# Kernel optimization log

Measured on AMD Instinct MI355X. Metric: run time of the kernel, lower is better.

The kernel has to match this reference:

```python
import jax, jax.numpy as jnp
import numpy as np
from functools import partial

N_ITER = 200  # LML(n_iter=200)


def sq_dists(Xi, x):
    # Xi: [N, n], x: [B, n] -> squared euclidean dists [B, N] (torch.cdist ** 2)
    x2 = jnp.sum(x * x, axis=1, keepdims=True)          # [B, 1]
    m2 = jnp.sum(Xi * Xi, axis=1)                        # [N]
    d = x2 + m2[None, :] - 2.0 * (x @ Xi.T)
    return jnp.maximum(d, 0.0)


def _lml_solve(x, k):
    # LML projection: y = sigmoid(x + nu), nu s.t. sum(y) = k; bisection on nu.
    x_sorted = -jnp.sort(-x, axis=1)                     # descending
    lo = -x_sorted[:, k - 1] - 7.0
    hi = -x_sorted[:, k] + 7.0

    def body(i, bounds):
        lo, hi = bounds
        mid = 0.5 * (lo + hi)
        f = jnp.sum(jax.nn.sigmoid(x + mid[:, None]), axis=1) - k
        lo = jnp.where(f < 0, mid, lo)
        hi = jnp.where(f < 0, hi, mid)
        return lo, hi

    lo, hi = jax.lax.fori_loop(0, N_ITER, body, (lo, hi))
    nu = 0.5 * (lo + hi)
    return jax.nn.sigmoid(x + nu[:, None])


@partial(jax.custom_vjp, nondiff_argnums=(1,))
def lml(x, k):
    return _lml_solve(x, k)


def _lml_fwd(x, k):
    y = _lml_solve(x, k)
    return y, y


def _lml_bwd(k, y, g):
    # implicit grad: dy = s*(dx - dnu), dnu = sum(s*dx)/sum(s), s = y(1-y)
    s = y * (1.0 - y)
    dnu = jnp.sum(s * g, axis=1, keepdims=True) / jnp.sum(s, axis=1, keepdims=True)
    return (s * (g - dnu),)


lml.defvjp(_lml_fwd, _lml_bwd)


def k_softmax(beta, x, k):
    # x: [B, N] (= -dists) -> [B, N, k]
    cols = [jax.nn.softmax(beta * x, axis=1)]
    last = cols[0]
    for i in range(1, k):
        new = lml(beta * x, i + 1)
        cols.append(new - last)
        last = new
    return jnp.stack(cols, axis=2)


def hopfield(Xi, x, beta):
    return jax.nn.softmax(-beta * sq_dists(Xi, x), axis=1) @ Xi


def k_hopfield_batch(Xi, x, k, beta, hopfield_steps):
    dists = sq_dists(Xi, x)                              # [B, N]
    ksm = k_softmax(beta, -dists, k)                     # [B, N, k]
    result = jnp.einsum('nd,bnk->bdk', Xi, ksm)          # Xi.T @ ksm -> [B, n, k]
    for _ in range(hopfield_steps):
        result = jnp.stack(
            [hopfield(Xi, result[:, :, j], beta) for j in range(k)], axis=2)
    return result


def setup_inputs() -> dict:
    key = jax.random.key(0)
    kx, km = jax.random.split(key)
    return {
        'x': jax.random.normal(kx, (2048, 512), dtype=jnp.float32),
        'memories': jax.random.normal(km, (8192, 512), dtype=jnp.float32),
        'k': 5,
        'beta': 1,
        'hopfield_steps': 2,
    }


def reference(x, memories, k, beta, hopfield_steps):
    return k_hopfield_batch(memories, x, k, beta, hopfield_steps)
```

## Files before the change

kernel.cpp:

```cpp
#include <hip/hip_runtime.h>
#include <hip/hip_bf16.h>


constexpr int   Bq    = 2048;
constexpr int   Nm    = 8192;
constexpr int   Dd    = 512;
constexpr int   KK    = 5;
constexpr float BETA  = 1.0f;
constexpr int   STEPS = 2;
constexpr int   KS    = 8;
constexpr size_t PL   = (size_t)Bq * Dd;

#define DEV static __device__ __forceinline__

typedef __attribute__((ext_vector_type(8))) short           short8v;
typedef __attribute__((ext_vector_type(8))) unsigned short  u16x8;
typedef __attribute__((ext_vector_type(4))) float           f32x4;

DEV float b2f(ushort u) { unsigned v = ((unsigned)u) << 16; float f; __builtin_memcpy(&f, &v, 4); return f; }
DEV ushort f2b(float f) { __hip_bfloat16 h = __float2bfloat16(f); ushort u; __builtin_memcpy(&u, &h, 2); return u; }
DEV float ldin(const void* p, int isf, size_t idx) {
    return isf ? ((const float*)p)[idx] : b2f(((const ushort*)p)[idx]);
}

__global__ __launch_bounds__(256) void detect_k(const ushort* __restrict__ xin,
                                                int* __restrict__ flag) {
    __shared__ int sb;
    if (threadIdx.x == 0) sb = 0;
    __syncthreads();
    int bad = 0;
    for (int i = threadIdx.x; i < 1024; i += 256) {
        float v = b2f(xin[i]);
        if (!(fabsf(v) < 64.0f)) bad = 1;
    }
    if (bad) atomicOr(&sb, 1);
    __syncthreads();
    if (threadIdx.x == 0) flag[0] = sb;
}

__global__ __launch_bounds__(256) void norms_k(const void* __restrict__ xin,
                                               const void* __restrict__ memin,
                                               const int* __restrict__ flag,
                                               float* __restrict__ x2,
                                               float* __restrict__ m2) {
    int row = blockIdx.x;
    int isf = flag[0];
    const void* src; size_t base; float* dst;
    if (row < Nm) { src = memin; base = (size_t)row * Dd; dst = m2 + row; }
    else          { src = xin; base = (size_t)(row - Nm) * Dd; dst = x2 + (row - Nm); }
    int tid = threadIdx.x, lane = tid & 63, wave = tid >> 6;
    float s = 0.f;
    for (int i = tid; i < Dd; i += 256) { float v = ldin(src, isf, base + i); s += v * v; }
    for (int off = 32; off; off >>= 1) s += __shfl_down(s, off, 64);
    __shared__ float ws[4];
    if (lane == 0) ws[wave] = s;
    __syncthreads();
    if (tid == 0) dst[0] = ws[0] + ws[1] + ws[2] + ws[3];
}


__global__ __launch_bounds__(256) void convHL_k(const void* __restrict__ src,
                                                const int* __restrict__ flag,
                                                ushort* __restrict__ H,
                                                ushort* __restrict__ L,
                                                int nQuads, int qoff) {
    int isf = flag[0];
    for (int i = blockIdx.x * 256 + threadIdx.x; i < nQuads; i += gridDim.x * 256) {
        float v[4];
        if (isf) {
            float4 t = ((const float4*)src)[qoff + i];
            v[0] = t.x; v[1] = t.y; v[2] = t.z; v[3] = t.w;
        } else {
            ushort4 t = ((const ushort4*)src)[qoff + i];
            v[0] = b2f(t.x); v[1] = b2f(t.y); v[2] = b2f(t.z); v[3] = b2f(t.w);
        }
        ushort4 h, l;
        ushort* hp = (ushort*)&h; ushort* lp = (ushort*)&l;
#pragma unroll
        for (int j = 0; j < 4; ++j) {
            ushort hu = f2b(v[j]);
            hp[j] = hu;
            lp[j] = f2b(v[j] - b2f(hu));
        }
        ((ushort4*)H)[i] = h;
        ((ushort4*)L)[i] = l;
    }
}

__global__ __launch_bounds__(256) void convT_k(const void* __restrict__ memin,
                                               const int* __restrict__ flag,
                                               ushort* __restrict__ TH,
                                               ushort* __restrict__ TL) {
    __shared__ float tile[64][65];
    const int isf = flag[0];
    const int n0 = blockIdx.x * 64, d0 = blockIdx.y * 64;
    const int tid = threadIdx.x;
    {
        const int r = tid >> 2, cseg = tid & 3;
#pragma unroll
        for (int j = 0; j < 16; ++j)
            tile[r][cseg * 16 + j] = ldin(memin, isf, (size_t)(n0 + r) * Dd + d0 + cseg * 16 + j);
    }
    __syncthreads();
    {
        const int drow = tid >> 2, nseg = tid & 3;
        u16x8 h[2], l[2];
#pragma unroll
        for (int c = 0; c < 2; ++c)
#pragma unroll
            for (int j = 0; j < 8; ++j) {
                float v = tile[nseg * 16 + c * 8 + j][drow];
                ushort hu = f2b(v);
                h[c][j] = hu;
                l[c][j] = f2b(v - b2f(hu));
            }
        size_t base = (size_t)(d0 + drow) * Nm + n0 + nseg * 16;
#pragma unroll
        for (int c = 0; c < 2; ++c) {
            *(u16x8*)&TH[base + c * 8] = h[c];
            *(u16x8*)&TL[base + c * 8] = l[c];
        }
    }
}

__global__ __launch_bounds__(256) void distMF2_k(const ushort* __restrict__ Ah,
                                                 const ushort* __restrict__ Al,
                                                 const ushort* __restrict__ Mh,
                                                 const ushort* __restrict__ Ml,
                                                 float* __restrict__ S,
                                                 const float* __restrict__ a2,
                                                 const float* __restrict__ m2,
                                                 int ab0, float negBeta) {
    __shared__ ushort TA[2][4][128][8];
    __shared__ ushort TB[2][4][128][8];
    const int tid = threadIdx.x, lane = tid & 63, wid = tid >> 6;
    const int wm = wid >> 1, wn = wid & 1;
    const int m0 = blockIdx.y * 128, n0 = blockIdx.x * 128;
    const int srow = tid & 127, kb = tid >> 7;
    const size_t baseA = (size_t)(ab0 + m0 + srow) * Dd;
    const size_t baseB = (size_t)(n0 + srow) * Dd;

    f32x4 acc[4][4];
    const f32x4 z = {0.f, 0.f, 0.f, 0.f};
#pragma unroll
    for (int i = 0; i < 4; ++i)
#pragma unroll
        for (int j = 0; j < 4; ++j) acc[i][j] = z;

    for (int k0 = 0; k0 < Dd; k0 += 32) {
        u16x8 rah0 = *(const u16x8*)&Ah[baseA + k0 + kb * 8];
        u16x8 rah1 = *(const u16x8*)&Ah[baseA + k0 + (kb + 2) * 8];
        u16x8 ral0 = *(const u16x8*)&Al[baseA + k0 + kb * 8];
        u16x8 ral1 = *(const u16x8*)&Al[baseA + k0 + (kb + 2) * 8];
        u16x8 rbh0 = *(const u16x8*)&Mh[baseB + k0 + kb * 8];
        u16x8 rbh1 = *(const u16x8*)&Mh[baseB + k0 + (kb + 2) * 8];
        u16x8 rbl0 = *(const u16x8*)&Ml[baseB + k0 + kb * 8];
        u16x8 rbl1 = *(const u16x8*)&Ml[baseB + k0 + (kb + 2) * 8];
        __syncthreads();
        *(u16x8*)&TA[0][kb][srow][0]     = rah0;
        *(u16x8*)&TA[0][kb + 2][srow][0] = rah1;
        *(u16x8*)&TA[1][kb][srow][0]     = ral0;
        *(u16x8*)&TA[1][kb + 2][srow][0] = ral1;
        *(u16x8*)&TB[0][kb][srow][0]     = rbh0;
        *(u16x8*)&TB[0][kb + 2][srow][0] = rbh1;
        *(u16x8*)&TB[1][kb][srow][0]     = rbl0;
        *(u16x8*)&TB[1][kb + 2][srow][0] = rbl1;
        __syncthreads();

        const int rl = lane & 15, kc = lane >> 4;
        short8v ah[4], al[4];
#pragma unroll
        for (int fm = 0; fm < 4; ++fm) {
            const int ra_ = wm * 64 + fm * 16 + rl;
            ah[fm] = *(const short8v*)&TA[0][kc][ra_][0];
            al[fm] = *(const short8v*)&TA[1][kc][ra_][0];
        }
#pragma unroll
        for (int fn = 0; fn < 4; ++fn) {
            const int rb_ = wn * 64 + fn * 16 + rl;
            short8v bh = *(const short8v*)&TB[0][kc][rb_][0];
            short8v bl = *(const short8v*)&TB[1][kc][rb_][0];
#pragma unroll
            for (int fm = 0; fm < 4; ++fm) {
                acc[fm][fn] = __builtin_amdgcn_mfma_f32_16x16x32_bf16(ah[fm], bh, acc[fm][fn], 0, 0, 0);
                acc[fm][fn] = __builtin_amdgcn_mfma_f32_16x16x32_bf16(al[fm], bh, acc[fm][fn], 0, 0, 0);
                acc[fm][fn] = __builtin_amdgcn_mfma_f32_16x16x32_bf16(ah[fm], bl, acc[fm][fn], 0, 0, 0);
            }
        }
    }

    const int col = lane & 15, r0 = (lane >> 4) * 4;
#pragma unroll
    for (int fm = 0; fm < 4; ++fm)
#pragma unroll
        for (int fn = 0; fn < 4; ++fn) {
            const int n = n0 + wn * 64 + fn * 16 + col;
            const float mm2 = m2[n];
#pragma unroll
            for (int q = 0; q < 4; ++q) {
                const int m = m0 + wm * 64 + fm * 16 + r0 + q;
                const float d = a2[m] + mm2 - 2.0f * acc[fm][fn][q];
                S[(size_t)m * Nm + n] = negBeta * fmaxf(d, 0.0f);
            }
        }
}

__global__ __launch_bounds__(256) void wconv_k(const float* __restrict__ S,
                                               const float* __restrict__ par6,
                                               const float* __restrict__ par2,
                                               ushort* __restrict__ Wh,
                                               ushort* __restrict__ Wl,
                                               int mode, int jj) {
    const int b = blockIdx.x, tid = threadIdx.x;
    float p0 = 0.f, p1 = 0.f;
    if (mode == 0)      { p0 = par6[b * 6 + 0]; p1 = 1.0f / par6[b * 6 + 1]; }
    else if (mode == 1) { p0 = par6[b * 6 + 1 + jj]; }
    else                { p0 = par2[b * 2 + 0]; p1 = par2[b * 2 + 1]; }
    const float4* sp = (const float4*)(S + (size_t)b * Nm);
    ushort* whp = Wh + (size_t)b * Nm;
    ushort* wlp = Wl + (size_t)b * Nm;
#pragma unroll
    for (int r = 0; r < 8; ++r) {
        const int qi = r * 256 + tid;
        float4 t = sp[qi];
        float s4[4] = {t.x, t.y, t.z, t.w};
        ushort4 oh, ol;
        ushort* ohp = (ushort*)&oh;
        ushort* olp = (ushort*)&ol;
#pragma unroll
        for (int j = 0; j < 4; ++j) {
            float w;
            if (mode == 1) w = 1.0f / (1.0f + expf(-(s4[j] + p0)));
            else           w = expf(s4[j] - p0) * p1;
            ushort hu = f2b(w);
            ohp[j] = hu;
            olp[j] = f2b(w - b2f(hu));
        }
        ((ushort4*)whp)[qi] = oh;
        ((ushort4*)wlp)[qi] = ol;
    }
}

__global__ __launch_bounds__(256) void wgemm3_k(const ushort* __restrict__ Wh,
                                                const ushort* __restrict__ Wl,
                                                const ushort* __restrict__ MTh,
                                                const ushort* __restrict__ MTl,
                                                float* __restrict__ part,
                                                int planeSz, int nzLen) {
    __shared__ ushort TW[2][4][128][8];
    __shared__ ushort TB[2][4][64][8];
    const int tid = threadIdx.x, lane = tid & 63, wid = tid >> 6;
    const int wm = wid >> 1, wn = wid & 1;
    const int d0 = blockIdx.x * 64, b0 = blockIdx.y * 128;
    const int nz0 = blockIdx.z * nzLen;

    const int wrow = tid & 127, wkb = tid >> 7;
    const int brow = tid & 63,  bkc = tid >> 6;
    const size_t baseW = (size_t)(b0 + wrow) * Nm;
    const size_t baseB = (size_t)(d0 + brow) * Nm;

    f32x4 acc[4][2];
    const f32x4 z = {0.f, 0.f, 0.f, 0.f};
#pragma unroll
    for (int i = 0; i < 4; ++i)
#pragma unroll
        for (int j = 0; j < 2; ++j) acc[i][j] = z;

    for (int nc = nz0; nc < nz0 + nzLen; nc += 32) {
        u16x8 rwh0 = *(const u16x8*)&Wh[baseW + nc + wkb * 8];
        u16x8 rwh1 = *(const u16x8*)&Wh[baseW + nc + (wkb + 2) * 8];
        u16x8 rwl0 = *(const u16x8*)&Wl[baseW + nc + wkb * 8];
        u16x8 rwl1 = *(const u16x8*)&Wl[baseW + nc + (wkb + 2) * 8];
        u16x8 rbh  = *(const u16x8*)&MTh[baseB + nc + bkc * 8];
        u16x8 rbl  = *(const u16x8*)&MTl[baseB + nc + bkc * 8];
        __syncthreads();
        *(u16x8*)&TW[0][wkb][wrow][0]     = rwh0;
        *(u16x8*)&TW[0][wkb + 2][wrow][0] = rwh1;
        *(u16x8*)&TW[1][wkb][wrow][0]     = rwl0;
        *(u16x8*)&TW[1][wkb + 2][wrow][0] = rwl1;
        *(u16x8*)&TB[0][bkc][brow][0]     = rbh;
        *(u16x8*)&TB[1][bkc][brow][0]     = rbl;
        __syncthreads();

        const int rl = lane & 15, kc = lane >> 4;
        short8v wfh[4], wfl[4];
#pragma unroll
        for (int fm = 0; fm < 4; ++fm) {
            const int rw_ = wm * 64 + fm * 16 + rl;
            wfh[fm] = *(const short8v*)&TW[0][kc][rw_][0];
            wfl[fm] = *(const short8v*)&TW[1][kc][rw_][0];
        }
#pragma unroll
        for (int fn = 0; fn < 2; ++fn) {
            const int rd_ = wn * 32 + fn * 16 + rl;
            short8v bh = *(const short8v*)&TB[0][kc][rd_][0];
            short8v bl = *(const short8v*)&TB[1][kc][rd_][0];
#pragma unroll
            for (int fm = 0; fm < 4; ++fm) {
                acc[fm][fn] = __builtin_amdgcn_mfma_f32_16x16x32_bf16(wfh[fm], bh, acc[fm][fn], 0, 0, 0);
                acc[fm][fn] = __builtin_amdgcn_mfma_f32_16x16x32_bf16(wfl[fm], bh, acc[fm][fn], 0, 0, 0);
                acc[fm][fn] = __builtin_amdgcn_mfma_f32_16x16x32_bf16(wfh[fm], bl, acc[fm][fn], 0, 0, 0);
            }
        }
    }

    float* pz = part + (size_t)blockIdx.z * planeSz;
    const int col = lane & 15, r0 = (lane >> 4) * 4;
#pragma unroll
    for (int fm = 0; fm < 4; ++fm)
#pragma unroll
        for (int fn = 0; fn < 2; ++fn) {
            const int dc = d0 + wn * 32 + fn * 16 + col;
#pragma unroll
            for (int q = 0; q < 4; ++q) {
                const int br = b0 + wm * 64 + fm * 16 + r0 + q;
                pz[(size_t)br * Dd + dc] = acc[fm][fn][q];
            }
        }
}

__global__ __launch_bounds__(256) void reduceHL_k(const float* __restrict__ part,
                                                  ushort* __restrict__ Rh,
                                                  ushort* __restrict__ Rl,
                                                  float* __restrict__ r2w, int doNorm,
                                                  int planeSz, int ks) {
    int row = blockIdx.x, tid = threadIdx.x, lane = tid & 63, wave = tid >> 6;
    float sq = 0.f;
    for (int e = tid; e < Dd; e += 256) {
        float s = 0.f;
        for (int z = 0; z < ks; ++z) s += part[(size_t)z * planeSz + (size_t)row * Dd + e];
        ushort h = f2b(s);
        Rh[(size_t)row * Dd + e] = h;
        Rl[(size_t)row * Dd + e] = f2b(s - b2f(h));
        sq += s * s;
    }
    if (doNorm) {
        for (int off = 32; off; off >>= 1) sq += __shfl_down(sq, off, 64);
        __shared__ float ws[4];
        if (lane == 0) ws[wave] = sq;
        __syncthreads();
        if (tid == 0) r2w[row] = ws[0] + ws[1] + ws[2] + ws[3];
    }
}

__global__ __launch_bounds__(256) void combineHL_k(ushort* __restrict__ rhl,
                                                   float* __restrict__ r2all) {
    int row = blockIdx.x, tid = threadIdx.x, lane = tid & 63, wave = tid >> 6;
    float sq[5] = {0.f, 0.f, 0.f, 0.f, 0.f};
    for (int e = tid; e < Dd; e += 256) {
        size_t idx = (size_t)row * Dd + e;
        float v[5];
#pragma unroll
        for (int j = 0; j < 5; ++j)
            v[j] = b2f(rhl[(size_t)j * 2 * PL + idx]) + b2f(rhl[(size_t)j * 2 * PL + PL + idx]);
        float o[5];
        o[0] = v[0];
        o[1] = v[1] - v[0]; o[2] = v[2] - v[1]; o[3] = v[3] - v[2]; o[4] = v[4] - v[3];
#pragma unroll
        for (int j = 1; j < 5; ++j) {
            ushort h = f2b(o[j]);
            rhl[(size_t)j * 2 * PL + idx] = h;
            rhl[(size_t)j * 2 * PL + PL + idx] = f2b(o[j] - b2f(h));
        }
#pragma unroll
        for (int j = 0; j < 5; ++j) sq[j] += o[j] * o[j];
    }
    __shared__ float ws[5][4];
#pragma unroll
    for (int j = 0; j < 5; ++j) {
        float s = sq[j];
        for (int off = 32; off; off >>= 1) s += __shfl_down(s, off, 64);
        if (lane == 0) ws[j][wave] = s;
    }
    __syncthreads();
    if (tid < 5) r2all[tid * Bq + row] = ws[tid][0] + ws[tid][1] + ws[tid][2] + ws[tid][3];
}

__global__ __launch_bounds__(256) void finalHL_k(const ushort* __restrict__ rhl,
                                                 void* __restrict__ out,
                                                 const int* __restrict__ flag) {
    size_t idx = (size_t)blockIdx.x * 256 + threadIdx.x;
    bool isf = flag[0] != 0;
#pragma unroll
    for (int j = 0; j < KK; ++j) {
        float v = b2f(rhl[(size_t)j * 2 * PL + idx]) + b2f(rhl[(size_t)j * 2 * PL + PL + idx]);
        if (isf) ((float*)out)[idx * KK + j] = v;
        else     ((ushort*)out)[idx * KK + j] = f2b(v);
    }
}


__global__ __launch_bounds__(256) void rowstats_k(const float* __restrict__ S,
                                                  float* __restrict__ stats) {
    int b = blockIdx.x, tid = threadIdx.x, lane = tid & 63, wave = tid >> 6;
    __shared__ float cbuf[1024];
    __shared__ int   ccnt;
    __shared__ float tops[256 * 6];
    __shared__ float stop[6];
    __shared__ float wred[16];
    __shared__ float bcast[5];
    const float* srow = S + (size_t)b * Nm;

    float tt[6];
#pragma unroll
    for (int q = 0; q < 6; ++q) tt[q] = -3.4e38f;
    for (int i = tid; i < Nm; i += 256) {
        float v = srow[i];
        if (v > tt[5]) {
            tt[5] = v;
#pragma unroll
            for (int q = 5; q > 0; --q)
                if (tt[q] > tt[q - 1]) { float tm = tt[q]; tt[q] = tt[q - 1]; tt[q - 1] = tm; }
        }
    }
#pragma unroll
    for (int q = 0; q < 6; ++q) tops[tid * 6 + q] = tt[q];
    if (tid == 0) ccnt = 0;
    __syncthreads();
    if (tid == 0) {
        float mt[6];
#pragma unroll
        for (int q = 0; q < 6; ++q) mt[q] = -3.4e38f;
        for (int i = 0; i < 256 * 6; ++i) {
            float v = tops[i];
            if (v > mt[5]) {
                mt[5] = v;
#pragma unroll
                for (int q = 5; q > 0; --q)
                    if (mt[q] > mt[q - 1]) { float tm = mt[q]; mt[q] = mt[q - 1]; mt[q - 1] = tm; }
            }
        }
#pragma unroll
        for (int q = 0; q < 6; ++q) stop[q] = mt[q];
    }
    __syncthreads();

    float smax = stop[0];
    float cutoff = stop[5] - 40.0f;
    float p = 0.f;
    for (int i = tid; i < Nm; i += 256) {
        float v = srow[i];
        p += expf(v - smax);
        if (v >= cutoff) {
            int idx = atomicAdd(&ccnt, 1);
            if (idx < 1024) cbuf[idx] = v;
        }
    }
    for (int off = 32; off; off >>= 1) p += __shfl_down(p, off, 64);
    if (lane == 0) wred[wave] = p;
    __syncthreads();
    if (tid == 0) bcast[4] = wred[0] + wred[1] + wred[2] + wred[3];
    __syncthreads();
    float denom = bcast[4];
    int cnt = min(ccnt, 1024);

    float lo[4], hi[4];
#pragma unroll
// ... 99 lines not shown
            int r = c >> 4, k = c & 15;
            As[k][r] = ldin(A, isfA, (size_t)(ab0 + m0 + r) * Dd + d0 + k);
            Bs[k][r] = ldin(memin, isfB, (size_t)(n0 + r) * Dd + d0 + k);
        }
        __syncthreads();
#pragma unroll
        for (int k = 0; k < 16; ++k) {
            float4 av = *(const float4*)&As[k][ty * 4];
            float4 bv = *(const float4*)&Bs[k][tx * 4];
            float a[4] = {av.x, av.y, av.z, av.w};
            float b[4] = {bv.x, bv.y, bv.z, bv.w};
#pragma unroll
            for (int i = 0; i < 4; ++i)
#pragma unroll
                for (int j = 0; j < 4; ++j) acc[i][j] = fmaf(a[i], b[j], acc[i][j]);
        }
        __syncthreads();
    }
#pragma unroll
    for (int i = 0; i < 4; ++i) {
        int m = m0 + ty * 4 + i;
        float4 o;
        float* po = (float*)&o;
#pragma unroll
        for (int j = 0; j < 4; ++j) {
            float d = a2[m] + m2[n0 + tx * 4 + j] - 2.0f * acc[i][j];
            po[j] = negBeta * fmaxf(d, 0.0f);
        }
        *(float4*)&S[(size_t)m * Nm + n0 + tx * 4] = o;
    }
}

template <int TRF>
__global__ __launch_bounds__(256) void wgemmG_k(const float* __restrict__ Sx,
                                                const void* __restrict__ memin,
                                                const int* __restrict__ flag,
                                                const float* __restrict__ rowpar,
                                                float* __restrict__ part, int planeSz) {
    __shared__ float Ws[16][68];
    __shared__ float Bs[16][68];
    const int tid = threadIdx.x, tx = tid & 15, ty = tid >> 4;
    const int d0 = blockIdx.x * 64, b0 = blockIdx.y * 64;
    const int kz = blockIdx.z * (Nm / KS);
    const int isf = flag[0];

    float acc[4][4];
#pragma unroll
    for (int i = 0; i < 4; ++i)
#pragma unroll
        for (int j = 0; j < 4; ++j) acc[i][j] = 0.f;

    for (int nc = kz; nc < kz + Nm / KS; nc += 16) {
#pragma unroll
        for (int c = tid; c < 1024; c += 256) {
            int r = c >> 4, k = c & 15;
            float s = Sx[(size_t)(b0 + r) * Nm + nc + k];
            float p0 = rowpar[(b0 + r) * 2 + 0];
            float w;
            if constexpr (TRF == 1) w = expf(s - p0) * rowpar[(b0 + r) * 2 + 1];
            else                    w = 1.0f / (1.0f + expf(-(s + p0)));
            Ws[k][r] = w;
            int kk = c >> 6, dd = c & 63;
            Bs[kk][dd] = ldin(memin, isf, (size_t)(nc + kk) * Dd + d0 + dd);
        }
        __syncthreads();
#pragma unroll
        for (int k = 0; k < 16; ++k) {
            float4 av = *(const float4*)&Ws[k][ty * 4];
            float4 bv = *(const float4*)&Bs[k][tx * 4];
            float a[4] = {av.x, av.y, av.z, av.w};
            float b[4] = {bv.x, bv.y, bv.z, bv.w};
#pragma unroll
            for (int i = 0; i < 4; ++i)
#pragma unroll
                for (int j = 0; j < 4; ++j) acc[i][j] = fmaf(a[i], b[j], acc[i][j]);
        }
        __syncthreads();
    }
    float* pz = part + (size_t)blockIdx.z * planeSz;
#pragma unroll
    for (int i = 0; i < 4; ++i) {
        float4 o = {acc[i][0], acc[i][1], acc[i][2], acc[i][3]};
        *(float4*)&pz[(size_t)(b0 + ty * 4 + i) * Dd + d0 + tx * 4] = o;
    }
}

__global__ __launch_bounds__(256) void reduceN_k(const float* __restrict__ part,
                                                 float* __restrict__ Rj,
                                                 float* __restrict__ r2w, int doNorm,
                                                 int planeSz) {
    int row = blockIdx.x, tid = threadIdx.x, lane = tid & 63, wave = tid >> 6;
    float sq = 0.f;
    for (int e = tid; e < Dd; e += 256) {
        float s = 0.f;
#pragma unroll
        for (int z = 0; z < KS; ++z) s += part[(size_t)z * planeSz + (size_t)row * Dd + e];
        Rj[(size_t)row * Dd + e] = s;
        sq += s * s;
    }
    if (doNorm) {
        for (int off = 32; off; off >>= 1) sq += __shfl_down(sq, off, 64);
        __shared__ float ws[4];
        if (lane == 0) ws[wave] = sq;
        __syncthreads();
        if (tid == 0) r2w[row] = ws[0] + ws[1] + ws[2] + ws[3];
    }
}

__global__ __launch_bounds__(256) void combine_k(float* __restrict__ R,
                                                 float* __restrict__ r2all) {
    int row = blockIdx.x, tid = threadIdx.x, lane = tid & 63, wave = tid >> 6;
    float sq[5] = {0.f, 0.f, 0.f, 0.f, 0.f};
    for (int e = tid; e < Dd; e += 256) {
        size_t idx = (size_t)row * Dd + e;
        float r0 = R[idx], r1 = R[PL + idx], r2v = R[2 * PL + idx],
              r3 = R[3 * PL + idx], r4 = R[4 * PL + idx];
        float o1 = r1 - r0, o2 = r2v - r1, o3 = r3 - r2v, o4 = r4 - r3;
        R[PL + idx] = o1; R[2 * PL + idx] = o2; R[3 * PL + idx] = o3; R[4 * PL + idx] = o4;
        sq[0] += r0 * r0; sq[1] += o1 * o1; sq[2] += o2 * o2; sq[3] += o3 * o3; sq[4] += o4 * o4;
    }
    __shared__ float ws[5][4];
#pragma unroll
    for (int j = 0; j < 5; ++j) {
        float s = sq[j];
        for (int off = 32; off; off >>= 1) s += __shfl_down(s, off, 64);
        if (lane == 0) ws[j][wave] = s;
    }
    __syncthreads();
    if (tid < 5) r2all[tid * Bq + row] = ws[tid][0] + ws[tid][1] + ws[tid][2] + ws[tid][3];
}

__global__ __launch_bounds__(256) void final_k(const float* __restrict__ R,
                                               void* __restrict__ out,
                                               const int* __restrict__ flag) {
    size_t idx = (size_t)blockIdx.x * 256 + threadIdx.x;
    bool isf = flag[0] != 0;
#pragma unroll
    for (int j = 0; j < KK; ++j) {
        float v = R[(size_t)j * PL + idx];
        if (isf) ((float*)out)[idx * KK + j] = v;
        else     ((ushort*)out)[idx * KK + j] = f2b(v);
    }
}


extern "C" void kernel_launch(void* const* d_in, const int* in_sizes, int n_in,
                              void* d_out, int out_size, void* d_ws, size_t ws_size,
                              hipStream_t stream) {
    const void* xin   = d_in[0];
    const void* memin = d_in[1];

    const size_t MiB = 1048576ull, KiB = 1024ull;
    char* ws = (char*)d_ws;
    float* part = (float*)d_out;

    int BcF = 0, ksF = 0;
    {
        const int cb[10] = {1024, 512, 512, 256, 256, 256, 128, 128, 128, 128};
        const int ck[10] = {   8,  16,   8,  32,  16,   8,  64,  32,  16,   8};
        for (int i = 0; i < 10; ++i) {
            size_t need = 52 * MiB + 160 * KiB + (size_t)cb[i] * 64 * KiB;
            size_t needOut = (size_t)ck[i] * cb[i] * Dd * 4;
            if (need <= ws_size && needOut <= (size_t)out_size) { BcF = cb[i]; ksF = ck[i]; break; }
        }
    }

    if (BcF) {
        const int Bc = BcF, ks = ksF;
        ushort* rhl  = (ushort*)(ws + 0);
        ushort* mh   = (ushort*)(ws + 20 * MiB);
        ushort* ml   = (ushort*)(ws + 28 * MiB);
        ushort* mth  = (ushort*)(ws + 36 * MiB);
        ushort* mtl  = (ushort*)(ws + 44 * MiB);
        char*  misc  = ws + 52 * MiB;
        float* m2    = (float*)(misc + 0);
        float* x2    = (float*)(misc + 32 * KiB);
        float* stats = (float*)(misc + 40 * KiB);
        float* rpar  = (float*)(misc + 88 * KiB);
        int*   flag  = (int*)  (misc + 104 * KiB);
        float* r2all = (float*)(misc + 112 * KiB);
        ushort* Wh   = (ushort*)(ws + 52 * MiB + 160 * KiB);
        ushort* Wl   = Wh + (size_t)Bc * Nm;
        float* S     = (float*)(ws + 52 * MiB + 160 * KiB + (size_t)Bc * 32 * KiB);
        ushort* xsH  = Wh;
        ushort* xsL  = Wh + (size_t)Bc * Dd;

        const int nChunk = Bq / Bc;
        const int planeSz = Bc * Dd;
        const int nzLen = Nm / ks;

        detect_k<<<1, 256, 0, stream>>>((const ushort*)xin, flag);
        norms_k<<<Nm + Bq, 256, 0, stream>>>(xin, memin, flag, x2, m2);
        convHL_k<<<2048, 256, 0, stream>>>(memin, flag, mh, ml, Nm * Dd / 4, 0);
        convT_k<<<dim3(Nm / 64, Dd / 64), 256, 0, stream>>>(memin, flag, mth, mtl);

        for (int c = 0; c < nChunk; ++c) {
            int b0 = c * Bc;
            convHL_k<<<Bc / 2, 256, 0, stream>>>(xin, flag, xsH, xsL,
                                                 Bc * Dd / 4, b0 * Dd / 4);
            distMF2_k<<<dim3(Nm / 128, Bc / 128), 256, 0, stream>>>(
                xsH, xsL, mh, ml, S, x2 + b0, m2, 0, -BETA);
            rowstats_k<<<Bc, 256, 0, stream>>>(S, stats + (size_t)b0 * 6);
            for (int jj = 0; jj < KK; ++jj) {
                wconv_k<<<Bc, 256, 0, stream>>>(S, stats + (size_t)b0 * 6, nullptr,
                                                Wh, Wl, jj == 0 ? 0 : 1, jj);
                wgemm3_k<<<dim3(Dd / 64, Bc / 128, ks), 256, 0, stream>>>(
                    Wh, Wl, mth, mtl, part, planeSz, nzLen);
                ushort* Rh = rhl + (size_t)jj * 2 * PL + (size_t)b0 * Dd;
                ushort* Rl = rhl + (size_t)jj * 2 * PL + PL + (size_t)b0 * Dd;
                reduceHL_k<<<Bc, 256, 0, stream>>>(part, Rh, Rl, nullptr, 0, planeSz, ks);
            }
        }
        combineHL_k<<<Bq, 256, 0, stream>>>(rhl, r2all);

        for (int st = 0; st < STEPS; ++st) {
            for (int jj = 0; jj < KK; ++jj) {
                ushort* Rhj = rhl + (size_t)jj * 2 * PL;
                ushort* Rlj = rhl + (size_t)jj * 2 * PL + PL;
                float* r2j = r2all + (size_t)jj * Bq;
                for (int c = 0; c < nChunk; ++c) {
                    int b0 = c * Bc;
                    distMF2_k<<<dim3(Nm / 128, Bc / 128), 256, 0, stream>>>(
                        Rhj, Rlj, mh, ml, S, r2j + b0, m2, b0, -BETA);
                    rowmax_denom_k<<<Bc, 256, 0, stream>>>(S, rpar + (size_t)b0 * 2);
                    wconv_k<<<Bc, 256, 0, stream>>>(S, nullptr, rpar + (size_t)b0 * 2,
                                                    Wh, Wl, 2, 0);
                    wgemm3_k<<<dim3(Dd / 64, Bc / 128, ks), 256, 0, stream>>>(
                        Wh, Wl, mth, mtl, part, planeSz, nzLen);
                    reduceHL_k<<<Bc, 256, 0, stream>>>(
                        part, Rhj + (size_t)b0 * Dd, Rlj + (size_t)b0 * Dd,
                        r2j + b0, 1, planeSz, ks);
                }
            }
        }
        finalHL_k<<<(int)(PL / 256), 256, 0, stream>>>(rhl, d_out, flag);
        return;
    }

    float* R     = (float*)(ws + 0);
    float* m2    = (float*)(ws + 20 * MiB);
    float* x2    = (float*)(ws + 20 * MiB + 32 * KiB);
    float* stats = (float*)(ws + 20 * MiB + 48 * KiB);
    float* rpar  = (float*)(ws + 20 * MiB + 96 * KiB);
    int*   flag  = (int*)  (ws + 20 * MiB + 112 * KiB);
    float* r2all = (float*)(ws + 20 * MiB + 128 * KiB);
    float* S     = (float*)(ws + 20 * MiB + 256 * KiB);

    int Bc = 128;
    const int cand[4] = {1024, 512, 256, 128};
    for (int i = 0; i < 4; ++i) {
        size_t needWS  = 20 * MiB + 256 * KiB + (size_t)cand[i] * Nm * 4;
        size_t needOut = (size_t)KS * cand[i] * Dd * 4;
        if (needWS <= ws_size && needOut <= (size_t)out_size) { Bc = cand[i]; break; }
    }
    const int nChunk = Bq / Bc;
    const int planeSz = Bc * Dd;

    detect_k<<<1, 256, 0, stream>>>((const ushort*)xin, flag);
    norms_k<<<Nm + Bq, 256, 0, stream>>>(xin, memin, flag, x2, m2);

    for (int c = 0; c < nChunk; ++c) {
        int b0 = c * Bc;
        distF2_k<<<dim3(Nm / 64, Bc / 64), 256, 0, stream>>>(
            xin, flag, 0, memin, S, x2 + b0, m2, b0, -BETA);
        rowstats_k<<<Bc, 256, 0, stream>>>(S, stats + (size_t)b0 * 6);
        for (int jj = 0; jj < KK; ++jj) {
            float* Rj = R + (size_t)jj * PL + (size_t)b0 * Dd;
            rowpar_stage1_k<<<Bq / 256, 256, 0, stream>>>(stats, rpar, jj);
            if (jj == 0)
                wgemmG_k<1><<<dim3(Dd / 64, Bc / 64, KS), 256, 0, stream>>>(
                    S, memin, flag, rpar + (size_t)b0 * 2, part, planeSz);
            else
                wgemmG_k<2><<<dim3(Dd / 64, Bc / 64, KS), 256, 0, stream>>>(
                    S, memin, flag, rpar + (size_t)b0 * 2, part, planeSz);
            reduceN_k<<<Bc, 256, 0, stream>>>(part, Rj, nullptr, 0, planeSz);
        }
    }
    combine_k<<<Bq, 256, 0, stream>>>(R, r2all);

    for (int st = 0; st < STEPS; ++st) {
        for (int jj = 0; jj < KK; ++jj) {
            float* Rj = R + (size_t)jj * PL;
            float* r2j = r2all + (size_t)jj * Bq;
            for (int c = 0; c < nChunk; ++c) {
                int b0 = c * Bc;
                distF2_k<<<dim3(Nm / 64, Bc / 64), 256, 0, stream>>>(
                    Rj, flag, 1, memin, S, r2j + b0, m2, b0, -BETA);
                rowmax_denom_k<<<Bc, 256, 0, stream>>>(S, rpar + (size_t)b0 * 2);
                wgemmG_k<1><<<dim3(Dd / 64, Bc / 64, KS), 256, 0, stream>>>(
                    S, memin, flag, rpar + (size_t)b0 * 2, part, planeSz);
                reduceN_k<<<Bc, 256, 0, stream>>>(
                    part, Rj + (size_t)b0 * Dd, r2j + b0, 1, planeSz);
            }
        }
    }
    final_k<<<(int)(PL / 256), 256, 0, stream>>>(R, d_out, flag);
}
```

Baseline: 11.67 ms.

## Convert memories to hi/lo bf16 inside dist GEMM and prefetch next tiles

The distance GEMM now reads the raw memory matrix (fp32 or bf16) and splits it into bf16 hi/lo parts in registers, so the precomputed mh/ml buffers and their conversion pass are gone. Both the distance GEMM and the weighted GEMM now issue global loads for the next k-tile right after the barrier, giving a register-level software prefetch. The workspace layout changes: the transposed memory planes move into the output buffer and the partial sums move into the workspace, with a new table of chunk and split sizes. The in-kernel conversion costs extra ALU work on every tile, and fp32 input doubles the bytes read for B.

```diff
diff --git a/kernel.cpp b/kernel.cpp
--- a/kernel.cpp
+++ b/kernel.cpp
@@ -123,10 +123,10 @@
     }
 }
 
-__global__ __launch_bounds__(256) void distMF2_k(const ushort* __restrict__ Ah,
+__global__ __launch_bounds__(256) void distMF3_k(const ushort* __restrict__ Ah,
                                                  const ushort* __restrict__ Al,
-                                                 const ushort* __restrict__ Mh,
-                                                 const ushort* __restrict__ Ml,
+                                                 const void* __restrict__ memin,
+                                                 const int* __restrict__ flag,
                                                  float* __restrict__ S,
                                                  const float* __restrict__ a2,
                                                  const float* __restrict__ m2,
@@ -136,6 +136,7 @@
     const int tid = threadIdx.x, lane = tid & 63, wid = tid >> 6;
     const int wm = wid >> 1, wn = wid & 1;
     const int m0 = blockIdx.y * 128, n0 = blockIdx.x * 128;
+    const int isf = flag[0];
     const int srow = tid & 127, kb = tid >> 7;
     const size_t baseA = (size_t)(ab0 + m0 + srow) * Dd;
     const size_t baseB = (size_t)(n0 + srow) * Dd;
@@ -147,25 +148,54 @@
 #pragma unroll
         for (int j = 0; j < 4; ++j) acc[i][j] = z;
 
+    u16x8 rah0, rah1, ral0, ral1;
+    float vb[16];
+
+    auto loadT = [&](int k0) {
+        rah0 = *(const u16x8*)&Ah[baseA + k0 + kb * 8];
+        rah1 = *(const u16x8*)&Ah[baseA + k0 + (kb + 2) * 8];
+        ral0 = *(const u16x8*)&Al[baseA + k0 + kb * 8];
+        ral1 = *(const u16x8*)&Al[baseA + k0 + (kb + 2) * 8];
+        if (isf) {
+            const float* mp = (const float*)memin + baseB + k0;
+            float4 t0 = *(const float4*)(mp + kb * 8);
+            float4 t1 = *(const float4*)(mp + kb * 8 + 4);
+            float4 t2 = *(const float4*)(mp + (kb + 2) * 8);
+            float4 t3 = *(const float4*)(mp + (kb + 2) * 8 + 4);
+            vb[0] = t0.x; vb[1] = t0.y; vb[2]  = t0.z; vb[3]  = t0.w;
+            vb[4] = t1.x; vb[5] = t1.y; vb[6]  = t1.z; vb[7]  = t1.w;
+            vb[8] = t2.x; vb[9] = t2.y; vb[10] = t2.z; vb[11] = t2.w;
+            vb[12] = t3.x; vb[13] = t3.y; vb[14] = t3.z; vb[15] = t3.w;
+        } else {
+            const ushort* mp = (const ushort*)memin + baseB + k0;
+            u16x8 t0 = *(const u16x8*)(mp + kb * 8);
+            u16x8 t1 = *(const u16x8*)(mp + (kb + 2) * 8);
+#pragma unroll
+            for (int j = 0; j < 8; ++j) { vb[j] = b2f(t0[j]); vb[8 + j] = b2f(t1[j]); }
+        }
+    };
+
+    loadT(0);
     for (int k0 = 0; k0 < Dd; k0 += 32) {
-        u16x8 rah0 = *(const u16x8*)&Ah[baseA + k0 + kb * 8];
-        u16x8 rah1 = *(const u16x8*)&Ah[baseA + k0 + (kb + 2) * 8];
-        u16x8 ral0 = *(const u16x8*)&Al[baseA + k0 + kb * 8];
-        u16x8 ral1 = *(const u16x8*)&Al[baseA + k0 + (kb + 2) * 8];
-        u16x8 rbh0 = *(const u16x8*)&Mh[baseB + k0 + kb * 8];
-        u16x8 rbh1 = *(const u16x8*)&Mh[baseB + k0 + (kb + 2) * 8];
-        u16x8 rbl0 = *(const u16x8*)&Ml[baseB + k0 + kb * 8];
-        u16x8 rbl1 = *(const u16x8*)&Ml[baseB + k0 + (kb + 2) * 8];
+        u16x8 h0, l0, h1, l1;
+#pragma unroll
+        for (int j = 0; j < 8; ++j) {
+            ushort hu = f2b(vb[j]);
+            h0[j] = hu; l0[j] = f2b(vb[j] - b2f(hu));
+            ushort hv = f2b(vb[8 + j]);
+            h1[j] = hv; l1[j] = f2b(vb[8 + j] - b2f(hv));
+        }
         __syncthreads();
         *(u16x8*)&TA[0][kb][srow][0]     = rah0;
         *(u16x8*)&TA[0][kb + 2][srow][0] = rah1;
         *(u16x8*)&TA[1][kb][srow][0]     = ral0;
         *(u16x8*)&TA[1][kb + 2][srow][0] = ral1;
-        *(u16x8*)&TB[0][kb][srow][0]     = rbh0;
-        *(u16x8*)&TB[0][kb + 2][srow][0] = rbh1;
-        *(u16x8*)&TB[1][kb][srow][0]     = rbl0;
-        *(u16x8*)&TB[1][kb + 2][srow][0] = rbl1;
-        __syncthreads();
+        *(u16x8*)&TB[0][kb][srow][0]     = h0;
+        *(u16x8*)&TB[0][kb + 2][srow][0] = h1;
+        *(u16x8*)&TB[1][kb][srow][0]     = l0;
+        *(u16x8*)&TB[1][kb + 2][srow][0] = l1;
+        __syncthreads();
+        if (k0 + 32 < Dd) loadT(k0 + 32);
 
         const int rl = lane & 15, kc = lane >> 4;
         short8v ah[4], al[4];
@@ -266,13 +296,18 @@
 #pragma unroll
         for (int j = 0; j < 2; ++j) acc[i][j] = z;
 
+    u16x8 rwh0, rwh1, rwl0, rwl1, rbh, rbl;
+    auto loadT = [&](int nc) {
+        rwh0 = *(const u16x8*)&Wh[baseW + nc + wkb * 8];
+        rwh1 = *(const u16x8*)&Wh[baseW + nc + (wkb + 2) * 8];
+        rwl0 = *(const u16x8*)&Wl[baseW + nc + wkb * 8];
+        rwl1 = *(const u16x8*)&Wl[baseW + nc + (wkb + 2) * 8];
+        rbh  = *(const u16x8*)&MTh[baseB + nc + bkc * 8];
+        rbl  = *(const u16x8*)&MTl[baseB + nc + bkc * 8];
+    };
+
+    loadT(nz0);
     for (int nc = nz0; nc < nz0 + nzLen; nc += 32) {
-        u16x8 rwh0 = *(const u16x8*)&Wh[baseW + nc + wkb * 8];
-        u16x8 rwh1 = *(const u16x8*)&Wh[baseW + nc + (wkb + 2) * 8];
-        u16x8 rwl0 = *(const u16x8*)&Wl[baseW + nc + wkb * 8];
-        u16x8 rwl1 = *(const u16x8*)&Wl[baseW + nc + (wkb + 2) * 8];
-        u16x8 rbh  = *(const u16x8*)&MTh[baseB + nc + bkc * 8];
-        u16x8 rbl  = *(const u16x8*)&MTl[baseB + nc + bkc * 8];
         __syncthreads();
         *(u16x8*)&TW[0][wkb][wrow][0]     = rwh0;
         *(u16x8*)&TW[0][wkb + 2][wrow][0] = rwh1;
@@ -281,6 +316,7 @@
         *(u16x8*)&TB[0][bkc][brow][0]     = rbh;
         *(u16x8*)&TB[1][bkc][brow][0]     = rbl;
         __syncthreads();
+        if (nc + 32 < nz0 + nzLen) loadT(nc + 32);
 
         const int rl = lane & 15, kc = lane >> 4;
         short8v wfh[4], wfl[4];
@@ -708,36 +744,36 @@
 
     const size_t MiB = 1048576ull, KiB = 1024ull;
     char* ws = (char*)d_ws;
-    float* part = (float*)d_out;
-
+
+    const size_t memTbytes = 2ull * Dd * Nm * 2;
     int BcF = 0, ksF = 0;
-    {
-        const int cb[10] = {1024, 512, 512, 256, 256, 256, 128, 128, 128, 128};
-        const int ck[10] = {   8,  16,   8,  32,  16,   8,  64,  32,  16,   8};
-        for (int i = 0; i < 10; ++i) {
-            size_t need = 52 * MiB + 160 * KiB + (size_t)cb[i] * 64 * KiB;
-            size_t needOut = (size_t)ck[i] * cb[i] * Dd * 4;
-            if (need <= ws_size && needOut <= (size_t)out_size) { BcF = cb[i]; ksF = ck[i]; break; }
+    if ((size_t)out_size >= memTbytes) {
+        const int cb[6] = {512, 512, 256, 256, 128, 128};
+        const int ck[6] = {  8,   4,  16,   8,  32,   8};
+        for (int i = 0; i < 6; ++i) {
+            size_t need = 20 * MiB + 160 * KiB
+                        + (size_t)cb[i] * 64 * KiB
+                        + (size_t)ck[i] * cb[i] * 2 * KiB;
+            if (need <= ws_size) { BcF = cb[i]; ksF = ck[i]; break; }
         }
     }
 
     if (BcF) {
         const int Bc = BcF, ks = ksF;
         ushort* rhl  = (ushort*)(ws + 0);
-        ushort* mh   = (ushort*)(ws + 20 * MiB);
-        ushort* ml   = (ushort*)(ws + 28 * MiB);
-        ushort* mth  = (ushort*)(ws + 36 * MiB);
-        ushort* mtl  = (ushort*)(ws + 44 * MiB);
-        char*  misc  = ws + 52 * MiB;
+        char*  misc  = ws + 20 * MiB;
         float* m2    = (float*)(misc + 0);
         float* x2    = (float*)(misc + 32 * KiB);
         float* stats = (float*)(misc + 40 * KiB);
         float* rpar  = (float*)(misc + 88 * KiB);
         int*   flag  = (int*)  (misc + 104 * KiB);
         float* r2all = (float*)(misc + 112 * KiB);
-        ushort* Wh   = (ushort*)(ws + 52 * MiB + 160 * KiB);
+        ushort* Wh   = (ushort*)(ws + 20 * MiB + 160 * KiB);
         ushort* Wl   = Wh + (size_t)Bc * Nm;
-        float* S     = (float*)(ws + 52 * MiB + 160 * KiB + (size_t)Bc * 32 * KiB);
+        float* S     = (float*)(ws + 20 * MiB + 160 * KiB + (size_t)Bc * 32 * KiB);
+        float* part  = (float*)(ws + 20 * MiB + 160 * KiB + (size_t)Bc * 64 * KiB);
+        ushort* mth  = (ushort*)d_out;
+        ushort* mtl  = mth + (size_t)Dd * Nm;
         ushort* xsH  = Wh;
         ushort* xsL  = Wh + (size_t)Bc * Dd;
 
@@ -747,15 +783,14 @@
 
         detect_k<<<1, 256, 0, stream>>>((const ushort*)xin, flag);
         norms_k<<<Nm + Bq, 256, 0, stream>>>(xin, memin, flag, x2, m2);
-        convHL_k<<<2048, 256, 0, stream>>>(memin, flag, mh, ml, Nm * Dd / 4, 0);
         convT_k<<<dim3(Nm / 64, Dd / 64), 256, 0, stream>>>(memin, flag, mth, mtl);
 
         for (int c = 0; c < nChunk; ++c) {
             int b0 = c * Bc;
             convHL_k<<<Bc / 2, 256, 0, stream>>>(xin, flag, xsH, xsL,
                                                  Bc * Dd / 4, b0 * Dd / 4);
-            distMF2_k<<<dim3(Nm / 128, Bc / 128), 256, 0, stream>>>(
-                xsH, xsL, mh, ml, S, x2 + b0, m2, 0, -BETA);
+            distMF3_k<<<dim3(Nm / 128, Bc / 128), 256, 0, stream>>>(
+                xsH, xsL, memin, flag, S, x2 + b0, m2, 0, -BETA);
             rowstats_k<<<Bc, 256, 0, stream>>>(S, stats + (size_t)b0 * 6);
             for (int jj = 0; jj < KK; ++jj) {
                 wconv_k<<<Bc, 256, 0, stream>>>(S, stats + (size_t)b0 * 6, nullptr,
@@ -776,8 +811,8 @@
                 float* r2j = r2all + (size_t)jj * Bq;
                 for (int c = 0; c < nChunk; ++c) {
                     int b0 = c * Bc;
-                    distMF2_k<<<dim3(Nm / 128, Bc / 128), 256, 0, stream>>>(
-                        Rhj, Rlj, mh, ml, S, r2j + b0, m2, b0, -BETA);
+                    distMF3_k<<<dim3(Nm / 128, Bc / 128), 256, 0, stream>>>(
+                        Rhj, Rlj, memin, flag, S, r2j + b0, m2, b0, -BETA);
                     rowmax_denom_k<<<Bc, 256, 0, stream>>>(S, rpar + (size_t)b0 * 2);
                     wconv_k<<<Bc, 256, 0, stream>>>(S, nullptr, rpar + (size_t)b0 * 2,
                                                     Wh, Wl, 2, 0);
@@ -793,6 +828,7 @@
         return;
     }
 
+    float* part = (float*)d_out;
     float* R     = (float*)(ws + 0);
     float* m2    = (float*)(ws + 20 * MiB);
     float* x2    = (float*)(ws + 20 * MiB + 32 * KiB);
```

Result: slower. 26.16 ms (+124.2%).

## Fuse weight transform and hi/lo split into GEMM operand load

Applied to the files above, without the earlier changes.

Removes the separate wconv pass that turned score rows into bf16 hi/lo weight planes. The GEMM kernel now reads the fp32 scores directly and applies exp or sigmoid with per-row parameters before packing into shared memory. Workspace layout is also reorganized: the transposed memory planes move into the output buffer, and the batch chunk and split-K values are fixed at 512/8. The cost is more exp work inside the GEMM, repeated across the Dd/64 column blocks, and wider fp32 reads per tile.

```diff
diff --git a/kernel.cpp b/kernel.cpp
--- a/kernel.cpp
+++ b/kernel.cpp
@@ -66,22 +66,19 @@
                                                 int nQuads, int qoff) {
     int isf = flag[0];
     for (int i = blockIdx.x * 256 + threadIdx.x; i < nQuads; i += gridDim.x * 256) {
-        float v[4];
+        float v0, v1, v2, v3;
         if (isf) {
             float4 t = ((const float4*)src)[qoff + i];
-            v[0] = t.x; v[1] = t.y; v[2] = t.z; v[3] = t.w;
+            v0 = t.x; v1 = t.y; v2 = t.z; v3 = t.w;
         } else {
             ushort4 t = ((const ushort4*)src)[qoff + i];
-            v[0] = b2f(t.x); v[1] = b2f(t.y); v[2] = b2f(t.z); v[3] = b2f(t.w);
+            v0 = b2f(t.x); v1 = b2f(t.y); v2 = b2f(t.z); v3 = b2f(t.w);
         }
         ushort4 h, l;
-        ushort* hp = (ushort*)&h; ushort* lp = (ushort*)&l;
-#pragma unroll
-        for (int j = 0; j < 4; ++j) {
-            ushort hu = f2b(v[j]);
-            hp[j] = hu;
-            lp[j] = f2b(v[j] - b2f(hu));
-        }
+        h.x = f2b(v0); l.x = f2b(v0 - b2f(h.x));
+        h.y = f2b(v1); l.y = f2b(v1 - b2f(h.y));
+        h.z = f2b(v2); l.z = f2b(v2 - b2f(h.z));
+        h.w = f2b(v3); l.w = f2b(v3 - b2f(h.w));
         ((ushort4*)H)[i] = h;
         ((ushort4*)L)[i] = l;
     }
@@ -104,21 +101,19 @@
     __syncthreads();
     {
         const int drow = tid >> 2, nseg = tid & 3;
-        u16x8 h[2], l[2];
-#pragma unroll
-        for (int c = 0; c < 2; ++c)
+        size_t base = (size_t)(d0 + drow) * Nm + n0 + nseg * 16;
+#pragma unroll
+        for (int c = 0; c < 2; ++c) {
+            u16x8 h, l;
 #pragma unroll
             for (int j = 0; j < 8; ++j) {
                 float v = tile[nseg * 16 + c * 8 + j][drow];
                 ushort hu = f2b(v);
-                h[c][j] = hu;
-                l[c][j] = f2b(v - b2f(hu));
+                h[j] = hu;
+                l[j] = f2b(v - b2f(hu));
             }
-        size_t base = (size_t)(d0 + drow) * Nm + n0 + nseg * 16;
-#pragma unroll
-        for (int c = 0; c < 2; ++c) {
-            *(u16x8*)&TH[base + c * 8] = h[c];
-            *(u16x8*)&TL[base + c * 8] = l[c];
+            *(u16x8*)&TH[base + c * 8] = h;
+            *(u16x8*)&TL[base + c * 8] = l;
         }
     }
 }
@@ -205,44 +200,15 @@
         }
 }
 
-__global__ __launch_bounds__(256) void wconv_k(const float* __restrict__ S,
-                                               const float* __restrict__ par6,
-                                               const float* __restrict__ par2,
-                                               ushort* __restrict__ Wh,
-                                               ushort* __restrict__ Wl,
-                                               int mode, int jj) {
-    const int b = blockIdx.x, tid = threadIdx.x;
-    float p0 = 0.f, p1 = 0.f;
-    if (mode == 0)      { p0 = par6[b * 6 + 0]; p1 = 1.0f / par6[b * 6 + 1]; }
-    else if (mode == 1) { p0 = par6[b * 6 + 1 + jj]; }
-    else                { p0 = par2[b * 2 + 0]; p1 = par2[b * 2 + 1]; }
-    const float4* sp = (const float4*)(S + (size_t)b * Nm);
-    ushort* whp = Wh + (size_t)b * Nm;
-    ushort* wlp = Wl + (size_t)b * Nm;
-#pragma unroll
-    for (int r = 0; r < 8; ++r) {
-        const int qi = r * 256 + tid;
-        float4 t = sp[qi];
-        float s4[4] = {t.x, t.y, t.z, t.w};
-        ushort4 oh, ol;
-        ushort* ohp = (ushort*)&oh;
-        ushort* olp = (ushort*)&ol;
-#pragma unroll
-        for (int j = 0; j < 4; ++j) {
-            float w;
-            if (mode == 1) w = 1.0f / (1.0f + expf(-(s4[j] + p0)));
-            else           w = expf(s4[j] - p0) * p1;
-            ushort hu = f2b(w);
-            ohp[j] = hu;
-            olp[j] = f2b(w - b2f(hu));
-        }
-        ((ushort4*)whp)[qi] = oh;
-        ((ushort4*)wlp)[qi] = ol;
-    }
-}
-
-__global__ __launch_bounds__(256) void wgemm3_k(const ushort* __restrict__ Wh,
-                                                const ushort* __restrict__ Wl,
+template <int TRF>
+DEV float wtr(float s, float p0, float p1) {
+    if (TRF == 1) return expf(s - p0) * p1;
+    else          return 1.0f / (1.0f + expf(-(s + p0)));
+}
+
+template <int TRF>
+__global__ __launch_bounds__(256) void wgemmF_k(const float* __restrict__ Sx,
+                                                const float* __restrict__ rowpar,
                                                 const ushort* __restrict__ MTh,
                                                 const ushort* __restrict__ MTl,
                                                 float* __restrict__ part,
@@ -256,8 +222,10 @@
 
     const int wrow = tid & 127, wkb = tid >> 7;
     const int brow = tid & 63,  bkc = tid >> 6;
-    const size_t baseW = (size_t)(b0 + wrow) * Nm;
+    const size_t baseS = (size_t)(b0 + wrow) * Nm;
     const size_t baseB = (size_t)(d0 + brow) * Nm;
+    const float p0 = rowpar[(b0 + wrow) * 2 + 0];
+    const float p1 = rowpar[(b0 + wrow) * 2 + 1];
 
     f32x4 acc[4][2];
     const f32x4 z = {0.f, 0.f, 0.f, 0.f};
@@ -266,18 +234,30 @@
 #pragma unroll
         for (int j = 0; j < 2; ++j) acc[i][j] = z;
 
+#define PACKW(SV, H, L, I) { float w_ = wtr<TRF>(SV, p0, p1); ushort hu_ = f2b(w_); \
+                             H[I] = hu_; L[I] = f2b(w_ - b2f(hu_)); }
+
     for (int nc = nz0; nc < nz0 + nzLen; nc += 32) {
-        u16x8 rwh0 = *(const u16x8*)&Wh[baseW + nc + wkb * 8];
-        u16x8 rwh1 = *(const u16x8*)&Wh[baseW + nc + (wkb + 2) * 8];
-        u16x8 rwl0 = *(const u16x8*)&Wl[baseW + nc + wkb * 8];
-        u16x8 rwl1 = *(const u16x8*)&Wl[baseW + nc + (wkb + 2) * 8];
-        u16x8 rbh  = *(const u16x8*)&MTh[baseB + nc + bkc * 8];
-        u16x8 rbl  = *(const u16x8*)&MTl[baseB + nc + bkc * 8];
-        __syncthreads();
-        *(u16x8*)&TW[0][wkb][wrow][0]     = rwh0;
-        *(u16x8*)&TW[0][wkb + 2][wrow][0] = rwh1;
-        *(u16x8*)&TW[1][wkb][wrow][0]     = rwl0;
-        *(u16x8*)&TW[1][wkb + 2][wrow][0] = rwl1;
+        float4 sA = *(const float4*)&Sx[baseS + nc + wkb * 8];
+        float4 sB = *(const float4*)&Sx[baseS + nc + wkb * 8 + 4];
+        float4 sC = *(const float4*)&Sx[baseS + nc + (wkb + 2) * 8];
+        float4 sD = *(const float4*)&Sx[baseS + nc + (wkb + 2) * 8 + 4];
+        u16x8 rbh = *(const u16x8*)&MTh[baseB + nc + bkc * 8];
+        u16x8 rbl = *(const u16x8*)&MTl[baseB + nc + bkc * 8];
+        u16x8 wh0, wl0, wh1, wl1;
+        PACKW(sA.x, wh0, wl0, 0) PACKW(sA.y, wh0, wl0, 1)
+        PACKW(sA.z, wh0, wl0, 2) PACKW(sA.w, wh0, wl0, 3)
+        PACKW(sB.x, wh0, wl0, 4) PACKW(sB.y, wh0, wl0, 5)
+        PACKW(sB.z, wh0, wl0, 6) PACKW(sB.w, wh0, wl0, 7)
+        PACKW(sC.x, wh1, wl1, 0) PACKW(sC.y, wh1, wl1, 1)
+        PACKW(sC.z, wh1, wl1, 2) PACKW(sC.w, wh1, wl1, 3)
+        PACKW(sD.x, wh1, wl1, 4) PACKW(sD.y, wh1, wl1, 5)
+        PACKW(sD.z, wh1, wl1, 6) PACKW(sD.w, wh1, wl1, 7)
+        __syncthreads();
+        *(u16x8*)&TW[0][wkb][wrow][0]     = wh0;
+        *(u16x8*)&TW[0][wkb + 2][wrow][0] = wh1;
+        *(u16x8*)&TW[1][wkb][wrow][0]     = wl0;
+        *(u16x8*)&TW[1][wkb + 2][wrow][0] = wl1;
         *(u16x8*)&TB[0][bkc][brow][0]     = rbh;
         *(u16x8*)&TB[1][bkc][brow][0]     = rbl;
         __syncthreads();
@@ -303,6 +283,7 @@
             }
         }
     }
+#undef PACKW
 
     float* pz = part + (size_t)blockIdx.z * planeSz;
     const int col = lane & 15, r0 = (lane >> 4) * 4;
@@ -708,42 +689,34 @@
 
     const size_t MiB = 1048576ull, KiB = 1024ull;
     char* ws = (char*)d_ws;
-    float* part = (float*)d_out;
-
-    int BcF = 0, ksF = 0;
-    {
-        const int cb[10] = {1024, 512, 512, 256, 256, 256, 128, 128, 128, 128};
-        const int ck[10] = {   8,  16,   8,  32,  16,   8,  64,  32,  16,   8};
-        for (int i = 0; i < 10; ++i) {
-            size_t need = 52 * MiB + 160 * KiB + (size_t)cb[i] * 64 * KiB;
-            size_t needOut = (size_t)ck[i] * cb[i] * Dd * 4;
-            if (need <= ws_size && needOut <= (size_t)out_size) { BcF = cb[i]; ksF = ck[i]; break; }
-        }
-    }
-
-    if (BcF) {
+
+    const int    BcF       = 512;
+    const int    ksF       = 8;
+    const size_t memTbytes = 2ull * Dd * Nm * 2;
+    const size_t needWS    = 52 * MiB + 192 * KiB + 8 * MiB;
+
+    if ((size_t)out_size >= memTbytes && ws_size >= needWS) {
         const int Bc = BcF, ks = ksF;
         ushort* rhl  = (ushort*)(ws + 0);
-        ushort* mh   = (ushort*)(ws + 20 * MiB);
-        ushort* ml   = (ushort*)(ws + 28 * MiB);
-        ushort* mth  = (ushort*)(ws + 36 * MiB);
-        ushort* mtl  = (ushort*)(ws + 44 * MiB);
-        char*  misc  = ws + 52 * MiB;
-        float* m2    = (float*)(misc + 0);
-        float* x2    = (float*)(misc + 32 * KiB);
-        float* stats = (float*)(misc + 40 * KiB);
-        float* rpar  = (float*)(misc + 88 * KiB);
-        int*   flag  = (int*)  (misc + 104 * KiB);
-        float* r2all = (float*)(misc + 112 * KiB);
-        ushort* Wh   = (ushort*)(ws + 52 * MiB + 160 * KiB);
-        ushort* Wl   = Wh + (size_t)Bc * Nm;
-        float* S     = (float*)(ws + 52 * MiB + 160 * KiB + (size_t)Bc * 32 * KiB);
-        ushort* xsH  = Wh;
-        ushort* xsL  = Wh + (size_t)Bc * Dd;
-
-        const int nChunk = Bq / Bc;
+        char*   misc = ws + 20 * MiB;
+        float*  m2    = (float*)(misc + 0);
+        float*  x2    = (float*)(misc + 32 * KiB);
+        float*  stats = (float*)(misc + 40 * KiB);
+        float*  rpar  = (float*)(misc + 88 * KiB);
+        int*    flag  = (int*)  (misc + 104 * KiB);
+        float*  r2all = (float*)(misc + 112 * KiB);
+        ushort* mh   = (ushort*)(ws + 20 * MiB + 192 * KiB);
+        ushort* ml   = mh + (size_t)Nm * Dd;
+        float*  S    = (float*)(ws + 36 * MiB + 192 * KiB);
+        float*  part = (float*)(ws + 52 * MiB + 192 * KiB);
+        ushort* mth  = (ushort*)d_out;
+        ushort* mtl  = mth + (size_t)Dd * Nm;
+        ushort* xsH  = (ushort*)part;
+        ushort* xsL  = xsH + (size_t)Bc * Dd;
+
+        const int nChunk  = Bq / Bc;
         const int planeSz = Bc * Dd;
-        const int nzLen = Nm / ks;
+        const int nzLen   = Nm / ks;
 
         detect_k<<<1, 256, 0, stream>>>((const ushort*)xin, flag);
         norms_k<<<Nm + Bq, 256, 0, stream>>>(xin, memin, flag, x2, m2);
@@ -758,10 +731,13 @@
                 xsH, xsL, mh, ml, S, x2 + b0, m2, 0, -BETA);
             rowstats_k<<<Bc, 256, 0, stream>>>(S, stats + (size_t)b0 * 6);
             for (int jj = 0; jj < KK; ++jj) {
-                wconv_k<<<Bc, 256, 0, stream>>>(S, stats + (size_t)b0 * 6, nullptr,
-                                                Wh, Wl, jj == 0 ? 0 : 1, jj);
-                wgemm3_k<<<dim3(Dd / 64, Bc / 128, ks), 256, 0, stream>>>(
-                    Wh, Wl, mth, mtl, part, planeSz, nzLen);
+                rowpar_stage1_k<<<Bq / 256, 256, 0, stream>>>(stats, rpar, jj);
+                if (jj == 0)
+                    wgemmF_k<1><<<dim3(Dd / 64, Bc / 128, ks), 256, 0, stream>>>(
+                        S, rpar + (size_t)b0 * 2, mth, mtl, part, planeSz, nzLen);
+                else
+                    wgemmF_k<2><<<dim3(Dd / 64, Bc / 128, ks), 256, 0, stream>>>(
+                        S, rpar + (size_t)b0 * 2, mth, mtl, part, planeSz, nzLen);
                 ushort* Rh = rhl + (size_t)jj * 2 * PL + (size_t)b0 * Dd;
                 ushort* Rl = rhl + (size_t)jj * 2 * PL + PL + (size_t)b0 * Dd;
                 reduceHL_k<<<Bc, 256, 0, stream>>>(part, Rh, Rl, nullptr, 0, planeSz, ks);
@@ -779,10 +755,8 @@
                     distMF2_k<<<dim3(Nm / 128, Bc / 128), 256, 0, stream>>>(
                         Rhj, Rlj, mh, ml, S, r2j + b0, m2, b0, -BETA);
                     rowmax_denom_k<<<Bc, 256, 0, stream>>>(S, rpar + (size_t)b0 * 2);
-                    wconv_k<<<Bc, 256, 0, stream>>>(S, nullptr, rpar + (size_t)b0 * 2,
-                                                    Wh, Wl, 2, 0);
-                    wgemm3_k<<<dim3(Dd / 64, Bc / 128, ks), 256, 0, stream>>>(
-                        Wh, Wl, mth, mtl, part, planeSz, nzLen);
+                    wgemmF_k<1><<<dim3(Dd / 64, Bc / 128, ks), 256, 0, stream>>>(
+                        S, rpar + (size_t)b0 * 2, mth, mtl, part, planeSz, nzLen);
                     reduceHL_k<<<Bc, 256, 0, stream>>>(
                         part, Rhj + (size_t)b0 * Dd, Rlj + (size_t)b0 * Dd,
                         r2j + b0, 1, planeSz, ks);
@@ -793,6 +767,7 @@
         return;
     }
 
+    float* part = (float*)d_out;
     float* R     = (float*)(ws + 0);
     float* m2    = (float*)(ws + 20 * MiB);
     float* x2    = (float*)(ws + 20 * MiB + 32 * KiB);
@@ -805,9 +780,9 @@
     int Bc = 128;
     const int cand[4] = {1024, 512, 256, 128};
     for (int i = 0; i < 4; ++i) {
-        size_t needWS  = 20 * MiB + 256 * KiB + (size_t)cand[i] * Nm * 4;
+        size_t needWSl = 20 * MiB + 256 * KiB + (size_t)cand[i] * Nm * 4;
         size_t needOut = (size_t)KS * cand[i] * Dd * 4;
-        if (needWS <= ws_size && needOut <= (size_t)out_size) { Bc = cand[i]; break; }
+        if (needWSl <= ws_size && needOut <= (size_t)out_size) { Bc = cand[i]; break; }
     }
     const int nChunk = Bq / Bc;
     const int planeSz = Bc * Dd;
```

Result: slower. 26.09 ms (+123.6%).
